# Optimization experiments

Hardware: AMD Instinct MI355X
Metric: run time of the kernel (lower is better)

## Reference

```python
import jax, jax.numpy as jnp
import numpy as np

N, E = 50000, 800000
IN_DIM, HID, H1, H2, NCLS = 512, 64, 4, 1, 40
NEG_SLOPE = 0.2


def gat_conv(x, src, dst, W, att_src, att_dst, b, heads, ch):
    # x: [N, F_in]; W: [F_in, heads*ch]; att_*: [heads, ch]; b: [heads*ch]
    n = x.shape[0]
    h = (x @ W).reshape(n, heads, ch)                      # [N,H,C]
    a_s = jnp.einsum('nhc,hc->nh', h, att_src)             # [N,H]
    a_d = jnp.einsum('nhc,hc->nh', h, att_dst)             # [N,H]
    e = jax.nn.leaky_relu(a_s[src] + a_d[dst], NEG_SLOPE)  # [E,H]
    # segment softmax over incoming edges of each destination node
    m = jax.ops.segment_max(e, dst, num_segments=n)        # [N,H]
    ex = jnp.exp(e - m[dst])
    s = jax.ops.segment_sum(ex, dst, num_segments=n)       # [N,H]
    alpha = ex / (s[dst] + 1e-16)                          # [E,H]
    out = jax.ops.segment_sum(alpha[:, :, None] * h[src], dst, num_segments=n)
    return out.reshape(n, heads * ch) + b


def setup_inputs() -> dict:
    key = jax.random.key(0)
    ks = jax.random.split(key, 10)
    glorot = lambda k, shp: jax.random.normal(k, shp, jnp.float32) * jnp.sqrt(2.0 / (shp[0] + shp[-1]))
    return {
        'x': jax.random.normal(ks[0], (N, IN_DIM), jnp.float32),
        'edge_index': jax.random.randint(ks[1], (2, E), 0, N, jnp.int64),
        'W1': glorot(ks[2], (IN_DIM, H1 * HID)),
        'att_src1': glorot(ks[3], (H1, HID)),
        'att_dst1': glorot(ks[4], (H1, HID)),
        'b1': jnp.zeros((H1 * HID,), jnp.float32),
        'W2': glorot(ks[5], (H1 * HID, H2 * NCLS)),
        'att_src2': glorot(ks[6], (H2, NCLS)),
        'att_dst2': glorot(ks[7], (H2, NCLS)),
        'b2': jnp.zeros((H2 * NCLS,), jnp.float32),
    }


def reference(x, edge_index, W1, att_src1, att_dst1, b1, W2, att_src2, att_dst2, b2):
    n = x.shape[0]
    loops = jnp.arange(n, dtype=edge_index.dtype)
    src = jnp.concatenate([edge_index[0], loops])  # add self loops (PyG default)
    dst = jnp.concatenate([edge_index[1], loops])
    # dropout layers are identity in eval mode
    h = gat_conv(x, src, dst, W1, att_src1, att_dst1, b1, H1, HID)
    h = jax.nn.elu(h)
    out = gat_conv(h, src, dst, W2, att_src2, att_dst2, b2, H2, NCLS)
    return jax.nn.log_softmax(out, axis=1)
```

## Files before the change

kernel.cpp:

```cpp
#include <hip/hip_runtime.h>
#include <math.h>
#include <stdint.h>


typedef short bf16x8 __attribute__((ext_vector_type(8)));
typedef float f32x4  __attribute__((ext_vector_type(4)));

static __device__ __forceinline__ float leaky(float x){ return x > 0.f ? x : 0.2f*x; }
static __device__ __forceinline__ unsigned short f2bf(float f){
  uint32_t u = __float_as_uint(f);
  uint32_t r = u + 0x7fffu + ((u >> 16) & 1u);
  return (unsigned short)(r >> 16);
}
static __device__ __forceinline__ float bf2f(unsigned short u){
  return __uint_as_float(((uint32_t)u) << 16);
}

__global__ void k_cvt_w(const float* __restrict__ W, unsigned short* __restrict__ wt,
                        int* __restrict__ deg, int n){
  int i = blockIdx.x*blockDim.x + threadIdx.x;
  if (i < n) deg[i] = 0;
  if (i >= 512*256) return;
  int k = i >> 8, c = i & 255;
  wt[c*512 + k] = f2bf(W[i]);
}

__global__ void k_count(const int* __restrict__ ei, int E, int n, int* __restrict__ deg){
  int i = blockIdx.x*blockDim.x + threadIdx.x;
  int tot = E + n;
  if (i >= tot) return;
  int dst = (i < E) ? ei[E + i] : (i - E);
  atomicAdd(&deg[dst], 1);
}

__global__ __launch_bounds__(256) void k_scan_a(const int* __restrict__ deg,
    int* __restrict__ rowstart, int* __restrict__ bsum, int n){
  __shared__ int sm[256];
  int b = blockIdx.x, t = threadIdx.x;
  int i = b*256 + t;
  int v = (i < n) ? deg[i] : 0;
  sm[t] = v;
  __syncthreads();
  for (int off=1; off<256; off<<=1){
    int u = (t >= off) ? sm[t-off] : 0;
    __syncthreads();
    sm[t] += u;
    __syncthreads();
  }
  if (i < n) rowstart[i+1] = sm[t];
  if (t == 255) bsum[b] = sm[255];
}
__global__ __launch_bounds__(256) void k_scan_b(int* __restrict__ bsum, int nb){
  __shared__ int sm[256];
  int t = threadIdx.x;
  int v = (t < nb) ? bsum[t] : 0;
  sm[t] = v;
  __syncthreads();
  for (int off=1; off<256; off<<=1){
    int u = (t >= off) ? sm[t-off] : 0;
    __syncthreads();
    sm[t] += u;
    __syncthreads();
  }
  if (t < nb) bsum[t] = sm[t] - v;
}
__global__ __launch_bounds__(256) void k_scan_c(int* __restrict__ rowstart,
    const int* __restrict__ bsum, int* __restrict__ cur, int n){
  int b = blockIdx.x, t = threadIdx.x;
  int i = b*256 + t;
  if (i < n){ rowstart[i+1] += bsum[b]; cur[i] = 0; }
  if (i == 0) rowstart[0] = 0;
}

__global__ __launch_bounds__(256, 4) void k_gemm1_mfma(const float* __restrict__ X,
                                                    const unsigned short* __restrict__ BT,
                                                    const float* __restrict__ SW,
                                                    const float* __restrict__ DW,
                                                    unsigned short* __restrict__ Cb,
                                                    float* __restrict__ as1,
                                                    float* __restrict__ ad1, int M){
  __shared__ __align__(16) unsigned short lA[2][2048];
  __shared__ __align__(16) unsigned short lB[2][4096];
  const int t = threadIdx.x;
  const int lane = t & 63, w = t >> 6;
  const int wx = w & 1, wy = w >> 1;
  const int row0 = blockIdx.x * 64, col0 = blockIdx.y * 128;

  f32x4 acc[2][4];
  #pragma unroll
  for (int i=0;i<2;i++)
    #pragma unroll
    for (int j=0;j<4;j++)
      #pragma unroll
      for (int r=0;r<4;r++) acc[i][j][r] = 0.f;

  const int rA = t & 63, kqA = t >> 6;
  const float* xA = X + (size_t)min(row0 + rA, M-1)*512 + kqA*8;

  const int c0 = t, c1 = t + 256;
  const int rB0 = c0 & 127, kqB0 = c0 >> 7;
  const int rB1 = c1 & 127, kqB1 = c1 >> 7;
  const unsigned short* bB0 = BT + (size_t)(col0 + rB0)*512 + kqB0*8;
  const unsigned short* bB1 = BT + (size_t)(col0 + rB1)*512 + kqB1*8;

  const int kq = lane >> 4, li = lane & 15;

#define ISSUE_B(NXT, KTB) do{ \
  __builtin_amdgcn_global_load_lds((const __attribute__((address_space(1))) void*)(bB0 + (KTB)), \
      (__attribute__((address_space(3))) void*)&lB[NXT][c0*8], 16, 0, 0); \
  __builtin_amdgcn_global_load_lds((const __attribute__((address_space(1))) void*)(bB1 + (KTB)), \
      (__attribute__((address_space(3))) void*)&lB[NXT][c1*8], 16, 0, 0); }while(0)

#define CVT_WRITE(NXT, S0,S1) do{ \
  bf16x8 p0; \
  p0[0]=(short)f2bf(S0.x); p0[1]=(short)f2bf(S0.y); p0[2]=(short)f2bf(S0.z); p0[3]=(short)f2bf(S0.w); \
  p0[4]=(short)f2bf(S1.x); p0[5]=(short)f2bf(S1.y); p0[6]=(short)f2bf(S1.z); p0[7]=(short)f2bf(S1.w); \
  *(bf16x8*)&lA[NXT][t*8] = p0; }while(0)

#define STEP(T, CUR) do{ \
  float4 n0, n1; \
  if ((T) < 15){ \
    const int ktn = ((T)+1)*32; \
    n0 = *(const float4*)(xA + ktn); \
    n1 = *(const float4*)(xA + ktn + 4); \
    ISSUE_B((CUR)^1, ktn); \
  } \
  bf16x8 af[2], bfr[4]; \
  _Pragma("unroll") \
  for (int i=0;i<2;i++) \
    af[i]  = *(const bf16x8*)&lA[CUR][(kq*64 + wx*32 + i*16 + li)*8]; \
  _Pragma("unroll") \
  for (int j=0;j<4;j++) \
    bfr[j] = *(const bf16x8*)&lB[CUR][(kq*128 + wy*64 + j*16 + li)*8]; \
  _Pragma("unroll") \
  for (int i=0;i<2;i++) \
    _Pragma("unroll") \
    for (int j=0;j<4;j++) \
      acc[i][j] = __builtin_amdgcn_mfma_f32_16x16x32_bf16(af[i], bfr[j], acc[i][j], 0, 0, 0); \
  if ((T) < 15){ \
    CVT_WRITE((CUR)^1, n0, n1); \
    __syncthreads(); \
  } \
}while(0)

  {
    float4 a0 = *(const float4*)(xA);
    float4 a1 = *(const float4*)(xA + 4);
    ISSUE_B(0, 0);
    CVT_WRITE(0, a0, a1);
    __syncthreads();
  }

  #pragma unroll
  for (int tt = 0; tt < 8; ++tt){
    STEP(2*tt,   (0));
    STEP(2*tt+1, (1));
  }

#undef STEP
#undef CVT_WRITE
#undef ISSUE_B

  #pragma unroll
  for (int i=0;i<2;i++){
    #pragma unroll
    for (int r=0;r<4;r++){
      int row = row0 + wx*32 + i*16 + kq*4 + r;
      if (row < M){
        #pragma unroll
        for (int j=0;j<4;j++)
          Cb[(size_t)row*256 + col0 + wy*64 + j*16 + li] = f2bf(acc[i][j][r]);
      }
    }
  }

  const int hw = (int)blockIdx.y*2 + wy;
  float sv[4], dv[4];
  #pragma unroll
  for (int j=0;j<4;j++){
    sv[j] = SW[hw*64 + j*16 + li];
    dv[j] = DW[hw*64 + j*16 + li];
  }
  #pragma unroll
  for (int i=0;i<2;i++){
    #pragma unroll
    for (int r=0;r<4;r++){
      float ps = acc[i][0][r]*sv[0] + acc[i][1][r]*sv[1] + acc[i][2][r]*sv[2] + acc[i][3][r]*sv[3];
      float pd = acc[i][0][r]*dv[0] + acc[i][1][r]*dv[1] + acc[i][2][r]*dv[2] + acc[i][3][r]*dv[3];
      #pragma unroll
      for (int o=1;o<16;o<<=1){ ps += __shfl_xor(ps,o); pd += __shfl_xor(pd,o); }
      int row = row0 + wx*32 + i*16 + kq*4 + r;
      if (li == 0 && row < M){
        as1[row*4 + hw] = ps;
        ad1[row*4 + hw] = pd;
      }
    }
  }
}

__global__ void k_fill(const int* __restrict__ ei, int E, int n,
                       const int* __restrict__ rowstart, int* __restrict__ cur,
                       int* __restrict__ csr,
                       const float* __restrict__ as1, const float* __restrict__ ad1,
                       float* __restrict__ exbuf){
  int i = blockIdx.x*blockDim.x + threadIdx.x;
  int tot = E + n;
  if (i >= tot) return;
  int src, dst;
  if (i < E){ src = ei[i]; dst = ei[E+i]; } else { src = i - E; dst = src; }
  int pos = atomicAdd(&cur[dst], 1);
  int slot = rowstart[dst] + pos;
  csr[slot] = src;
  float4 a = *(const float4*)(as1 + (size_t)src*4);
  float4 d = *(const float4*)(ad1 + (size_t)dst*4);
  float4 ex;
  ex.x = __expf(fminf(leaky(a.x + d.x), 80.f));
  ex.y = __expf(fminf(leaky(a.y + d.y), 80.f));
  ex.z = __expf(fminf(leaky(a.z + d.z), 80.f));
  ex.w = __expf(fminf(leaky(a.w + d.w), 80.f));
  *(float4*)(exbuf + (size_t)slot*4) = ex;
}

__global__ __launch_bounds__(256) void k_agg1(const unsigned short* __restrict__ h1b,
    const float* __restrict__ exbuf,
    const int* __restrict__ rowstart, const int* __restrict__ csr,
    const float* __restrict__ b1, unsigned short* __restrict__ hactb, int n){
  int lane = threadIdx.x & 63;
  int node = blockIdx.x*4 + (threadIdx.x >> 6);
  if (node >= n) return;
  int lo = __builtin_amdgcn_readfirstlane(rowstart[node]);
  int hi = __builtin_amdgcn_readfirstlane(rowstart[node+1]);
  int h = lane >> 4;
  const float* exb = exbuf + h;
  float ax=0.f, ay=0.f, az=0.f, aw=0.f, psum=0.f;
  int e = lo;
  for (; e + 7 < hi; e += 8){
    int s0 = csr[e],   s1 = csr[e+1], s2 = csr[e+2], s3 = csr[e+3];
    int s4 = csr[e+4], s5 = csr[e+5], s6 = csr[e+6], s7 = csr[e+7];
    float e0 = exb[(size_t)e*4],     e1 = exb[(size_t)(e+1)*4],
          e2 = exb[(size_t)(e+2)*4], e3 = exb[(size_t)(e+3)*4],
          e4 = exb[(size_t)(e+4)*4], e5 = exb[(size_t)(e+5)*4],
          e6 = exb[(size_t)(e+6)*4], e7 = exb[(size_t)(e+7)*4];
    ushort4 u0 = *(const ushort4*)(h1b + (size_t)s0*256 + lane*4);
    ushort4 u1 = *(const ushort4*)(h1b + (size_t)s1*256 + lane*4);
    ushort4 u2 = *(const ushort4*)(h1b + (size_t)s2*256 + lane*4);
    ushort4 u3 = *(const ushort4*)(h1b + (size_t)s3*256 + lane*4);
    ushort4 u4 = *(const ushort4*)(h1b + (size_t)s4*256 + lane*4);
    ushort4 u5 = *(const ushort4*)(h1b + (size_t)s5*256 + lane*4);
    ushort4 u6 = *(const ushort4*)(h1b + (size_t)s6*256 + lane*4);
    ushort4 u7 = *(const ushort4*)(h1b + (size_t)s7*256 + lane*4);
    ax += e0*bf2f(u0.x) + e1*bf2f(u1.x) + e2*bf2f(u2.x) + e3*bf2f(u3.x)
        + e4*bf2f(u4.x) + e5*bf2f(u5.x) + e6*bf2f(u6.x) + e7*bf2f(u7.x);
    ay += e0*bf2f(u0.y) + e1*bf2f(u1.y) + e2*bf2f(u2.y) + e3*bf2f(u3.y)
        + e4*bf2f(u4.y) + e5*bf2f(u5.y) + e6*bf2f(u6.y) + e7*bf2f(u7.y);
    az += e0*bf2f(u0.z) + e1*bf2f(u1.z) + e2*bf2f(u2.z) + e3*bf2f(u3.z)
        + e4*bf2f(u4.z) + e5*bf2f(u5.z) + e6*bf2f(u6.z) + e7*bf2f(u7.z);
    aw += e0*bf2f(u0.w) + e1*bf2f(u1.w) + e2*bf2f(u2.w) + e3*bf2f(u3.w)
        + e4*bf2f(u4.w) + e5*bf2f(u5.w) + e6*bf2f(u6.w) + e7*bf2f(u7.w);
    psum += (e0+e1+e2+e3) + (e4+e5+e6+e7);
  }
  for (; e < hi; ++e){
    int s0 = csr[e];
    float e0 = exb[(size_t)e*4];
    ushort4 u0 = *(const ushort4*)(h1b + (size_t)s0*256 + lane*4);
    ax += e0*bf2f(u0.x); ay += e0*bf2f(u0.y); az += e0*bf2f(u0.z); aw += e0*bf2f(u0.w);
    psum += e0;
  }
  float inv = 1.f/(psum + 1e-16f);
  float4 bv = *(const float4*)(b1 + lane*4);
  float o0 = ax*inv + bv.x, o1 = ay*inv + bv.y, o2 = az*inv + bv.z, o3 = aw*inv + bv.w;
  ushort4 r;
  r.x = f2bf(o0 > 0.f ? o0 : expm1f(o0));
  r.y = f2bf(o1 > 0.f ? o1 : expm1f(o1));
  r.z = f2bf(o2 > 0.f ? o2 : expm1f(o2));
  r.w = f2bf(o3 > 0.f ? o3 : expm1f(o3));
  *(ushort4*)(hactb + (size_t)node*256 + lane*4) = r;
}

__global__ __launch_bounds__(256) void k_gemm2(const unsigned short* __restrict__ A,
    const float* __restrict__ B, const float* __restrict__ sw, const float* __restrict__ dw,
    unsigned short* __restrict__ Cb, float* __restrict__ as2, float* __restrict__ ad2, int M){
  __shared__ float Xl[32][129];
  __shared__ float Wl[128*40];
  __shared__ float Sps[32][8], Spd[32][8];
  int t = threadIdx.x;
  int row0 = blockIdx.x*32;
  int r = t & 31, g = t >> 5;
  float acc[5] = {0,0,0,0,0};
  for (int kt=0; kt<256; kt+=128){
    for (int i=t; i<1280; i+=256)
      *(float4*)&Wl[i*4] = *(const float4*)(B + kt*40 + i*4);
    for (int i=t; i<512; i+=256){
      int rr = i >> 4, k8 = i & 15;
      int grow = row0 + rr; if (grow >= M) grow = M-1;
      uint4 v = *(const uint4*)(A + (size_t)grow*256 + kt + k8*8);
      float* xp = &Xl[rr][k8*8];
      xp[0] = __uint_as_float(v.x << 16); xp[1] = __uint_as_float(v.x & 0xffff0000u);
      xp[2] = __uint_as_float(v.y << 16); xp[3] = __uint_as_float(v.y & 0xffff0000u);
      xp[4] = __uint_as_float(v.z << 16); xp[5] = __uint_as_float(v.z & 0xffff0000u);
      xp[6] = __uint_as_float(v.w << 16); xp[7] = __uint_as_float(v.w & 0xffff0000u);
    }
    __syncthreads();
    #pragma unroll 4
    for (int k=0;k<128;++k){
      float a = Xl[r][k];
      const float* wp = &Wl[k*40 + g*5];
      #pragma unroll
      for (int j=0;j<5;++j) acc[j] += a * wp[j];
    }
    __syncthreads();
  }
  int grow = row0 + r;
  float ps = 0.f, pd = 0.f;
  #pragma unroll
  for (int j=0;j<5;++j){
    ps += acc[j] * sw[g*5+j];
    pd += acc[j] * dw[g*5+j];
  }
  Sps[r][g] = ps; Spd[r][g] = pd;
  if (grow < M){
    #pragma unroll
    for (int j=0;j<5;++j) Cb[(size_t)grow*40 + g*5 + j] = f2bf(acc[j]);
  }
  __syncthreads();
  if (t < 32){
    float a = 0.f, b = 0.f;
    #pragma unroll
    for (int g2=0; g2<8; ++g2){ a += Sps[t][g2]; b += Spd[t][g2]; }
    int rw = row0 + t;
    if (rw < M){ as2[rw] = a; ad2[rw] = b; }
  }
}

__global__ __launch_bounds__(256) void k_pre2(const float* __restrict__ as2,
    const float* __restrict__ ad2, const int* __restrict__ rowstart,
    const int* __restrict__ csr, float* __restrict__ ex2, int n){
  int lane = threadIdx.x & 63;
  int node = blockIdx.x*4 + (threadIdx.x >> 6);
  if (node >= n) return;
  int lo = rowstart[node], hi = rowstart[node+1];
  float adn = ad2[node];
  for (int e = lo + lane; e < hi; e += 64)
    ex2[e] = __expf(fminf(leaky(as2[csr[e]] + adn), 80.f));
}

__global__ __launch_bounds__(256) void k_agg2(const unsigned short* __restrict__ h2b,
    const float* __restrict__ ex2,
    const int* __restrict__ rowstart, const int* __restrict__ csr,
    const float* __restrict__ b2, float* __restrict__ out, int n){
  int lane = threadIdx.x & 63;
  int node = blockIdx.x*4 + (threadIdx.x >> 6);
  if (node >= n) return;
  int lo = __builtin_amdgcn_readfirstlane(rowstart[node]);
  int hi = __builtin_amdgcn_readfirstlane(rowstart[node+1]);
  bool act = lane < 40;
  float acc = 0.f, psum = 0.f;
  int e = lo;
  for (; e + 7 < hi; e += 8){
    int s0 = csr[e],   s1 = csr[e+1], s2 = csr[e+2], s3 = csr[e+3];
    int s4 = csr[e+4], s5 = csr[e+5], s6 = csr[e+6], s7 = csr[e+7];
    float e0 = ex2[e],   e1 = ex2[e+1], e2 = ex2[e+2], e3 = ex2[e+3];
    float e4 = ex2[e+4], e5 = ex2[e+5], e6 = ex2[e+6], e7 = ex2[e+7];
    float h0 = act ? bf2f(h2b[(size_t)s0*40 + lane]) : 0.f;
    float h1 = act ? bf2f(h2b[(size_t)s1*40 + lane]) : 0.f;
    float h2 = act ? bf2f(h2b[(size_t)s2*40 + lane]) : 0.f;
    float h3 = act ? bf2f(h2b[(size_t)s3*40 + lane]) : 0.f;
    float h4 = act ? bf2f(h2b[(size_t)s4*40 + lane]) : 0.f;
    float h5 = act ? bf2f(h2b[(size_t)s5*40 + lane]) : 0.f;
    float h6 = act ? bf2f(h2b[(size_t)s6*40 + lane]) : 0.f;
    float h7 = act ? bf2f(h2b[(size_t)s7*40 + lane]) : 0.f;
    acc += e0*h0 + e1*h1 + e2*h2 + e3*h3 + e4*h4 + e5*h5 + e6*h6 + e7*h7;
    psum += (e0+e1+e2+e3) + (e4+e5+e6+e7);
  }
  for (; e < hi; ++e){
    int s0 = csr[e]; float e0 = ex2[e];
    acc += e0 * (act ? bf2f(h2b[(size_t)s0*40 + lane]) : 0.f);
    psum += e0;
  }
  float ov = acc/(psum + 1e-16f) + (act ? b2[lane] : 0.f);
  float v = act ? ov : -INFINITY;
  float mx = v;
  #pragma unroll
  for (int o=1;o<64;o<<=1) mx = fmaxf(mx, __shfl_xor(mx,o));
  float ev = act ? __expf(ov - mx) : 0.f;
  float se = ev;
  #pragma unroll
  for (int o=1;o<64;o<<=1) se += __shfl_xor(se,o);
  if (act) out[(size_t)node*40 + lane] = (ov - mx) - __logf(se);
}

extern "C" void kernel_launch(void* const* d_in, const int* in_sizes, int n_in,
                              void* d_out, int out_size, void* d_ws, size_t ws_size,
                              hipStream_t stream){
  const float* x   = (const float*)d_in[0];
  const int*   ei  = (const int*)d_in[1];
  const float* W1  = (const float*)d_in[2];
  const float* s1w = (const float*)d_in[3];
  const float* d1w = (const float*)d_in[4];
  const float* b1  = (const float*)d_in[5];
  const float* W2  = (const float*)d_in[6];
  const float* s2w = (const float*)d_in[7];
  const float* d2w = (const float*)d_in[8];
  const float* b2  = (const float*)d_in[9];
  float* out = (float*)d_out;

  const int N  = in_sizes[0] / 512;
  const int E  = in_sizes[1] / 2;
  const int Et = E + N;

  float* f = (float*)d_ws;
  unsigned short* h1b   = (unsigned short*)f;  f += (size_t)N*128;
  unsigned short* hactb = (unsigned short*)f;  f += (size_t)N*128;
  float* as1  = f;  f += (size_t)N*4;
  float* ad1  = f;  f += (size_t)N*4;
  float* as2  = f;  f += N;
  float* ad2  = f;  f += N;
  unsigned short* w1t = (unsigned short*)f;  f += 256*512/2;
  unsigned short* h2b = (unsigned short*)f;  f += (size_t)N*40/2 + 64;
  float* exbuf = f;  f += (size_t)Et*4;
  float* ex2   = f;  f += Et;
  int* ip = (int*)f;
  int* rowstart = ip;  ip += (N + 4) & ~3;
  int* deg      = ip;  ip += N;
  int* cur      = ip;  ip += N;
  int* csr      = ip;  ip += Et;
  int* bsum     = ip;  ip += 256;

  int nb4 = (N + 3) / 4;
  int nbs = (N + 255) / 256;
  k_cvt_w<<<512, 256, 0, stream>>>(W1, w1t, deg, N);
  k_count<<<(Et+255)/256, 256, 0, stream>>>(ei, E, N, deg);
  k_scan_a<<<nbs, 256, 0, stream>>>(deg, rowstart, bsum, N);
  k_scan_b<<<1, 256, 0, stream>>>(bsum, nbs);
  k_scan_c<<<nbs, 256, 0, stream>>>(rowstart, bsum, cur, N);
  k_gemm1_mfma<<<dim3((N+63)/64, 2), 256, 0, stream>>>(x, w1t, s1w, d1w, h1b, as1, ad1, N);
  k_fill <<<(Et+255)/256, 256, 0, stream>>>(ei, E, N, rowstart, cur, csr, as1, ad1, exbuf);
  k_agg1 <<<nb4, 256, 0, stream>>>(h1b, exbuf, rowstart, csr, b1, hactb, N);
  k_gemm2<<<(N+31)/32, 256, 0, stream>>>(hactb, W2, s2w, d2w, h2b, as2, ad2, N);
  k_pre2 <<<nb4, 256, 0, stream>>>(as2, ad2, rowstart, csr, ex2, N);
  k_agg2 <<<nb4, 256, 0, stream>>>(h2b, ex2, rowstart, csr, b2, out, N);
}
```

Measured before the change: 476.1 us.

## Pre-tile W1 into per-k-tile bf16 layout and coalesce GEMM1 A loads

The weight conversion kernel now writes W1 as bf16 in a [k-tile][k-quarter][column][8] layout, so each GEMM1 B-tile fetch reads one contiguous chunk instead of strided rows. The X loads are remapped so each wave reads 16 rows with four adjacent 32-byte chunks per row, which gives more coalesced global reads while keeping the same LDS layout. The occupancy hint in launch bounds is raised from 4 to 6, which may limit registers per thread, and the conversion kernel launches fewer blocks.

```diff
diff --git a/kernel.cpp b/kernel.cpp
--- a/kernel.cpp
+++ b/kernel.cpp
@@ -20,9 +20,14 @@
                         int* __restrict__ deg, int n){
   int i = blockIdx.x*blockDim.x + threadIdx.x;
   if (i < n) deg[i] = 0;
-  if (i >= 512*256) return;
-  int k = i >> 8, c = i & 255;
-  wt[c*512 + k] = f2bf(W[i]);
+  if (i >= 256*64) return;
+  int col = i & 255, kg = i >> 8;
+  int kt = kg >> 2, kq = kg & 3;
+  unsigned short* dst = wt + ((size_t)kt*1024 + kq*256 + col)*8;
+  bf16x8 p;
+  #pragma unroll
+  for (int j=0;j<8;j++) p[j] = (short)f2bf(W[(size_t)(kg*8+j)*256 + col]);
+  *(bf16x8*)dst = p;
 }
 
 __global__ void k_count(const int* __restrict__ ei, int E, int n, int* __restrict__ deg){
@@ -72,8 +77,8 @@
   if (i == 0) rowstart[0] = 0;
 }
 
-__global__ __launch_bounds__(256, 4) void k_gemm1_mfma(const float* __restrict__ X,
-                                                    const unsigned short* __restrict__ BT,
+__global__ __launch_bounds__(256, 6) void k_gemm1_mfma(const float* __restrict__ X,
+                                                    const unsigned short* __restrict__ WT,
                                                     const float* __restrict__ SW,
                                                     const float* __restrict__ DW,
                                                     unsigned short* __restrict__ Cb,
@@ -94,44 +99,43 @@
       #pragma unroll
       for (int r=0;r<4;r++) acc[i][j][r] = 0.f;
 
-  const int rA = t & 63, kqA = t >> 6;
-  const float* xA = X + (size_t)min(row0 + rA, M-1)*512 + kqA*8;
+  const int rA = w*16 + (lane & 15);
+  const int kA = lane >> 4;
+  const float* xA = X + (size_t)min(row0 + rA, M-1)*512 + kA*8;
+  const int aChunk = kA*64 + rA;
 
   const int c0 = t, c1 = t + 256;
-  const int rB0 = c0 & 127, kqB0 = c0 >> 7;
-  const int rB1 = c1 & 127, kqB1 = c1 >> 7;
-  const unsigned short* bB0 = BT + (size_t)(col0 + rB0)*512 + kqB0*8;
-  const unsigned short* bB1 = BT + (size_t)(col0 + rB1)*512 + kqB1*8;
-
-  const int kq = lane >> 4, li = lane & 15;
-
-#define ISSUE_B(NXT, KTB) do{ \
-  __builtin_amdgcn_global_load_lds((const __attribute__((address_space(1))) void*)(bB0 + (KTB)), \
+  const unsigned short* bB0 = WT + ((size_t)(c0>>7)*256 + col0 + (c0&127))*8;
+  const unsigned short* bB1 = WT + ((size_t)(c1>>7)*256 + col0 + (c1&127))*8;
+
+  const int fkq = lane >> 4, li = lane & 15;
+
+#define ISSUE_B(NXT, KT) do{ \
+  __builtin_amdgcn_global_load_lds((const __attribute__((address_space(1))) void*)(bB0 + (size_t)(KT)*8192), \
       (__attribute__((address_space(3))) void*)&lB[NXT][c0*8], 16, 0, 0); \
-  __builtin_amdgcn_global_load_lds((const __attribute__((address_space(1))) void*)(bB1 + (KTB)), \
+  __builtin_amdgcn_global_load_lds((const __attribute__((address_space(1))) void*)(bB1 + (size_t)(KT)*8192), \
       (__attribute__((address_space(3))) void*)&lB[NXT][c1*8], 16, 0, 0); }while(0)
 
 #define CVT_WRITE(NXT, S0,S1) do{ \
   bf16x8 p0; \
   p0[0]=(short)f2bf(S0.x); p0[1]=(short)f2bf(S0.y); p0[2]=(short)f2bf(S0.z); p0[3]=(short)f2bf(S0.w); \
   p0[4]=(short)f2bf(S1.x); p0[5]=(short)f2bf(S1.y); p0[6]=(short)f2bf(S1.z); p0[7]=(short)f2bf(S1.w); \
-  *(bf16x8*)&lA[NXT][t*8] = p0; }while(0)
+  *(bf16x8*)&lA[NXT][aChunk*8] = p0; }while(0)
 
 #define STEP(T, CUR) do{ \
   float4 n0, n1; \
   if ((T) < 15){ \
-    const int ktn = ((T)+1)*32; \
-    n0 = *(const float4*)(xA + ktn); \
-    n1 = *(const float4*)(xA + ktn + 4); \
-    ISSUE_B((CUR)^1, ktn); \
+    n0 = *(const float4*)(xA + ((T)+1)*32); \
+    n1 = *(const float4*)(xA + ((T)+1)*32 + 4); \
+    ISSUE_B((CUR)^1, (T)+1); \
   } \
   bf16x8 af[2], bfr[4]; \
   _Pragma("unroll") \
   for (int i=0;i<2;i++) \
-    af[i]  = *(const bf16x8*)&lA[CUR][(kq*64 + wx*32 + i*16 + li)*8]; \
+    af[i]  = *(const bf16x8*)&lA[CUR][(fkq*64 + wx*32 + i*16 + li)*8]; \
   _Pragma("unroll") \
   for (int j=0;j<4;j++) \
-    bfr[j] = *(const bf16x8*)&lB[CUR][(kq*128 + wy*64 + j*16 + li)*8]; \
+    bfr[j] = *(const bf16x8*)&lB[CUR][(fkq*128 + wy*64 + j*16 + li)*8]; \
   _Pragma("unroll") \
   for (int i=0;i<2;i++) \
     _Pragma("unroll") \
@@ -165,7 +169,7 @@
   for (int i=0;i<2;i++){
     #pragma unroll
     for (int r=0;r<4;r++){
-      int row = row0 + wx*32 + i*16 + kq*4 + r;
+      int row = row0 + wx*32 + i*16 + fkq*4 + r;
       if (row < M){
         #pragma unroll
         for (int j=0;j<4;j++)
@@ -189,7 +193,7 @@
       float pd = acc[i][0][r]*dv[0] + acc[i][1][r]*dv[1] + acc[i][2][r]*dv[2] + acc[i][3][r]*dv[3];
       #pragma unroll
       for (int o=1;o<16;o<<=1){ ps += __shfl_xor(ps,o); pd += __shfl_xor(pd,o); }
-      int row = row0 + wx*32 + i*16 + kq*4 + r;
+      int row = row0 + wx*32 + i*16 + fkq*4 + r;
       if (li == 0 && row < M){
         as1[row*4 + hw] = ps;
         ad1[row*4 + hw] = pd;
@@ -428,7 +432,7 @@
 
   int nb4 = (N + 3) / 4;
   int nbs = (N + 255) / 256;
-  k_cvt_w<<<512, 256, 0, stream>>>(W1, w1t, deg, N);
+  k_cvt_w<<<nbs, 256, 0, stream>>>(W1, w1t, deg, N);
   k_count<<<(Et+255)/256, 256, 0, stream>>>(ei, E, N, deg);
   k_scan_a<<<nbs, 256, 0, stream>>>(deg, rowstart, bsum, N);
   k_scan_b<<<1, 256, 0, stream>>>(bsum, nbs);
```

Result: faster. 456.9 us (-4.0%).
